# Kernel optimization log

Measured on AMD Instinct MI355X. Metric: run time of the kernel, lower is better.

## Reference

```python
import jax, jax.numpy as jnp
import numpy as np

WH, WW = 8, 8            # window_size
SH = 2                   # shuffle
NH = 6                   # num_heads
ED = 96                  # embed_dim
NP = WH * WW             # num_patches = 64
S2 = SH * SH             # shuffle group = 4
HD = ED // NH            # head_dim = 16
SCALE = HD ** -0.5 / SH
NW = 2048
NWM = 64
EPS = 1e-5


def _rel_pos_index():
    coords = np.stack(np.meshgrid(np.arange(WH), np.arange(WW), indexing='ij'))  # (2, wh, ww)
    cf = coords.reshape(2, -1)                                # (2, np)
    rel = (cf[:, :, None] - cf[:, None, :]).transpose(1, 2, 0).astype(np.int64)  # (np, np, 2)
    rel[..., 0] += WH - 1
    rel[..., 1] += WW - 1
    rel[..., 0] *= 2 * WW - 1
    return rel.sum(-1).reshape(-1)                            # (np*np,)

_REL_IDX = jnp.asarray(_rel_pos_index())


def setup_inputs() -> dict:
    key = jax.random.key(0)
    ks = jax.random.split(key, 6)
    return {
        'query': jax.random.normal(ks[0], (NW, NP * S2, ED), dtype=jnp.float32),
        'key': jax.random.normal(ks[1], (NW, NP * S2, ED), dtype=jnp.float32),
        'value': jax.random.normal(ks[2], (NW, NP * S2, ED), dtype=jnp.float32),
        'mask': jax.random.normal(ks[3], (NWM, NP, NP), dtype=jnp.float32),
        'bias_table': jax.random.normal(ks[4], (( 2 * WH - 1) * (2 * WW - 1), NH), dtype=jnp.float32) * 0.02,
        'norm_gamma': jnp.ones((S2, ED), dtype=jnp.float32),
        'norm_beta': jnp.zeros((S2, ED), dtype=jnp.float32),
        'proj_w': jax.random.normal(ks[5], (ED, ED), dtype=jnp.float32) * 0.02,
        'proj_b': jnp.zeros((ED,), dtype=jnp.float32),
    }


def reference(query, key, value, mask, bias_table, norm_gamma, norm_beta, proj_w, proj_b):
    nw = query.shape[0]

    def group(x):  # (nw, wh*sh*ww*sw, ed) -> (nw, np, s2, ed)
        x = x.reshape(nw, WH, SH, WW, SH, ED)
        return x.transpose(0, 1, 3, 2, 4, 5).reshape(nw, NP, S2, ED)

    q, k, v = group(query), group(key), group(value)

    # pre-norm LayerNorm over the joint (s2, ed) normalized shape
    mu = q.mean(axis=(-2, -1), keepdims=True)
    var = q.var(axis=(-2, -1), keepdims=True)
    q = (q - mu) / jnp.sqrt(var + EPS) * norm_gamma + norm_beta

    def heads(x):  # (nw, np, s2, ed) -> (nw, nh, np, s2, hd)
        return x.reshape(nw, NP, S2, NH, HD).transpose(0, 3, 1, 2, 4)

    q, k, v = heads(q), heads(k), heads(v)
    q = q * SCALE

    # QK^T contracting jointly over shuffle axis s and head_dim c
    attn = jnp.einsum('wnqsc,wnksc->wnqk', q, k)  # (nw, nh, np, np)

    bias = bias_table[_REL_IDX].reshape(NP, NP, NH).transpose(2, 0, 1)  # (nh, np, np)
    attn = attn + bias[None]

    nwm = mask.shape[0]
    b = nw // nwm
    attn = attn.reshape(b, nwm, NH, NP, NP) + mask[None, :, None]
    attn = jax.nn.softmax(attn.reshape(nw, NH, NP, NP), axis=-1)

    out = jnp.einsum('wnqk,wnksc->wnqsc', attn, v)  # (nw, nh, np, s2, hd)
    out = out.transpose(0, 2, 3, 1, 4).reshape(nw, NP, S2, ED)
    # group_partition_reversed
    out = out.reshape(nw, WH, WW, SH, SH, ED).transpose(0, 1, 3, 2, 4, 5).reshape(nw, NP * S2, ED)
    out = out @ proj_w.T + proj_b
    return out
```

## Files before the change

kernel.cpp:

```cpp
#include <hip/hip_runtime.h>
#include <hip/hip_bf16.h>


#define TPB 256

#define Q0   0
#define K0   8192
#define VT0  16384
#define PR0  24576
#define LDS_TOTAL 77824

typedef __attribute__((ext_vector_type(8))) short short8;
typedef __attribute__((ext_vector_type(4))) float f32x4;

union FRAG { uint4 u4; short8 s8; unsigned short us[8]; };

__device__ __forceinline__ int seq_of(int p, int s) {
    return ((p >> 3) << 5) | ((s >> 1) << 4) | ((p & 7) << 1) | (s & 1);
}

#define SWZ(row, slot) (((row) << 7) + ((((slot) ^ ((row) & 7))) << 4))

#define LGKM_FENCE() do { \
    asm volatile("s_waitcnt lgkmcnt(0)" ::: "memory"); \
    __builtin_amdgcn_sched_barrier(0); } while (0)

__device__ __forceinline__ unsigned short f2b(float x) {
    union { __hip_bfloat16 h; unsigned short u; } z;
    z.h = __float2bfloat16(x);
    return z.u;
}

__device__ __forceinline__ uint4 pack8(const float* v) {
    union { uint4 u4; unsigned short us[8]; } z;
#pragma unroll
    for (int i = 0; i < 8; ++i) z.us[i] = f2b(v[i]);
    return z.u4;
}

__device__ __forceinline__ void load_pack(const float* src, uint4* dst) {
    float v[16];
#pragma unroll
    for (int i = 0; i < 4; ++i) {
        float4 x = ((const float4*)src)[i];
        v[4 * i] = x.x; v[4 * i + 1] = x.y; v[4 * i + 2] = x.z; v[4 * i + 3] = x.w;
    }
    dst[0] = pack8(v);
    dst[1] = pack8(v + 8);
}

__global__ void build_comb(const float* __restrict__ gmask,
                           const float* __restrict__ gbt,
                           float* __restrict__ comb) {
    const int b = blockIdx.x;
    const int mi = b / 6, n = b - mi * 6;
    const int t = threadIdx.x;
    const float* mrow = gmask + (size_t)mi * 4096;
    float* crow = comb + (size_t)b * 4096;
#pragma unroll
    for (int e = 0; e < 4096; e += TPB) {
        const int i = e + t;
        const int q = i >> 6, k = i & 63;
        const int idx = ((q >> 3) - (k >> 3) + 7) * 15 + ((q & 7) - (k & 7) + 7);
        crow[i] = mrow[i] + gbt[idx * 6 + n];
    }
}

template <int USE_COMB>
__global__ __launch_bounds__(TPB, 2)
void dwa_mfma(const float* __restrict__ gq,
              const float* __restrict__ gk,
              const float* __restrict__ gv,
              const float* __restrict__ gmask,
              const float* __restrict__ gbt,
              const float* __restrict__ ggamma,
              const float* __restrict__ gbeta,
              const float* __restrict__ gpw,
              const float* __restrict__ gpb,
              float* __restrict__ gout,
              const float* __restrict__ comb,
              int nwm)
{
    __shared__ __align__(16) unsigned char Lraw[LDS_TOTAL];
    char* L = (char*)Lraw;

    const int w = blockIdx.x;
    const int t = threadIdx.x;
    const int lane = t & 63, wv = t >> 6;
    const int r15 = lane & 15, gsl = lane >> 4;

    const int p_a = t >> 2, s_a = t & 3;
    const int g_a = seq_of(p_a, s_a);
    const size_t rowbase = ((size_t)w * 256 + g_a) * 96;
    const int mbase = (w % nwm) * 4096;
    const int qr0 = (wv << 4) + (gsl << 2);
    const f32x4 zf = {0.f, 0.f, 0.f, 0.f};

    uint4 qreg[12];
    {
        float qv[96];
        float sum = 0.f, ssq = 0.f;
        const float4* qr4 = (const float4*)(gq + rowbase);
#pragma unroll
        for (int i = 0; i < 24; ++i) {
            float4 x = qr4[i];
            qv[4 * i] = x.x; qv[4 * i + 1] = x.y;
            qv[4 * i + 2] = x.z; qv[4 * i + 3] = x.w;
            sum += (x.x + x.y) + (x.z + x.w);
            ssq += (x.x * x.x + x.y * x.y) + (x.z * x.z + x.w * x.w);
        }
        sum += __shfl_xor(sum, 1); ssq += __shfl_xor(ssq, 1);
        sum += __shfl_xor(sum, 2); ssq += __shfl_xor(ssq, 2);
        const float mu = sum * (1.f / 384.f);
        const float rs = rsqrtf(ssq * (1.f / 384.f) - mu * mu + 1e-5f);
        const float4* ga4 = (const float4*)(ggamma + s_a * 96);
        const float4* be4 = (const float4*)(gbeta + s_a * 96);
#pragma unroll
        for (int c6 = 0; c6 < 6; ++c6) {
            float vals[16];
#pragma unroll
            for (int j = 0; j < 4; ++j) {
                float4 g = ga4[c6 * 4 + j];
                float4 b = be4[c6 * 4 + j];
                const int base = c6 * 16 + 4 * j;
                vals[4 * j + 0] = ((qv[base + 0] - mu) * rs * g.x + b.x) * 0.125f;
                vals[4 * j + 1] = ((qv[base + 1] - mu) * rs * g.y + b.y) * 0.125f;
                vals[4 * j + 2] = ((qv[base + 2] - mu) * rs * g.z + b.z) * 0.125f;
                vals[4 * j + 3] = ((qv[base + 3] - mu) * rs * g.w + b.w) * 0.125f;
            }
            qreg[2 * c6]     = pack8(vals);
            qreg[2 * c6 + 1] = pack8(vals + 8);
        }
    }

    uint4 kpf[2][2], vpf[2][2];
    load_pack(gk + rowbase, kpf[0]);
    load_pack(gv + rowbase, vpf[0]);

#pragma unroll
    for (int n = 0; n < 6; ++n) {
        *(uint4*)(L + Q0 + SWZ(p_a, s_a * 2))     = qreg[2 * n];
        *(uint4*)(L + Q0 + SWZ(p_a, s_a * 2 + 1)) = qreg[2 * n + 1];
        *(uint4*)(L + K0 + SWZ(p_a, s_a * 2))     = kpf[n & 1][0];
        *(uint4*)(L + K0 + SWZ(p_a, s_a * 2 + 1)) = kpf[n & 1][1];
#pragma unroll
        for (int h = 0; h < 2; ++h) {
            FRAG u; u.u4 = vpf[n & 1][h];
#pragma unroll
            for (int c = 0; c < 8; ++c) {
                const int np_ = s_a * 16 + h * 8 + c;
                *(unsigned short*)(L + VT0 + (np_ << 7) +
                    ((((p_a >> 3) ^ (np_ & 7))) << 4) + ((p_a & 7) << 1)) = u.us[c];
            }
        }
        if (n < 5) {
            load_pack(gk + rowbase + (n + 1) * 16, kpf[(n + 1) & 1]);
            load_pack(gv + rowbase + (n + 1) * 16, vpf[(n + 1) & 1]);
        }
        f32x4 sacc[4];
        if (USE_COMB) {
            const float* cb = comb + (size_t)((w % nwm) * 6 + n) * 4096;
#pragma unroll
            for (int tile = 0; tile < 4; ++tile)
#pragma unroll
                for (int r = 0; r < 4; ++r)
                    sacc[tile][r] = cb[((qr0 + r) << 6) + (tile << 4) + r15];
        } else {
#pragma unroll
            for (int tile = 0; tile < 4; ++tile) {
                const int kpx = (tile << 4) + r15;
                const int ik = kpx >> 3, jk = kpx & 7;
#pragma unroll
                for (int r = 0; r < 4; ++r) {
                    const int q = qr0 + r;
                    sacc[tile][r] = gbt[(((q >> 3) - ik + 7) * 15 + ((q & 7) - jk + 7)) * 6 + n]
                                  + gmask[mbase + (q << 6) + kpx];
                }
            }
        }
        __syncthreads();

        {
            FRAG a0, a1;
            a0.u4 = *(const uint4*)(L + Q0 + SWZ(wv * 16 + r15, gsl));
            a1.u4 = *(const uint4*)(L + Q0 + SWZ(wv * 16 + r15, 4 + gsl));
#pragma unroll
            for (int tile = 0; tile < 4; ++tile) {
                FRAG b0, b1;
                b0.u4 = *(const uint4*)(L + K0 + SWZ(tile * 16 + r15, gsl));
                b1.u4 = *(const uint4*)(L + K0 + SWZ(tile * 16 + r15, 4 + gsl));
                sacc[tile] = __builtin_amdgcn_mfma_f32_16x16x32_bf16(a0.s8, b0.s8, sacc[tile], 0, 0, 0);
                sacc[tile] = __builtin_amdgcn_mfma_f32_16x16x32_bf16(a1.s8, b1.s8, sacc[tile], 0, 0, 0);
            }
        }

#pragma unroll
        for (int r = 0; r < 4; ++r) {
            const int q = qr0 + r;
            float mx = fmaxf(fmaxf(sacc[0][r], sacc[1][r]),
                             fmaxf(sacc[2][r], sacc[3][r]));
            mx = fmaxf(mx, __shfl_xor(mx, 1));
            mx = fmaxf(mx, __shfl_xor(mx, 2));
            mx = fmaxf(mx, __shfl_xor(mx, 4));
            mx = fmaxf(mx, __shfl_xor(mx, 8));
            float sm = 0.f;
#pragma unroll
            for (int tile = 0; tile < 4; ++tile) {
                sacc[tile][r] = __expf(sacc[tile][r] - mx);
                sm += sacc[tile][r];
            }
            sm += __shfl_xor(sm, 1);
            sm += __shfl_xor(sm, 2);
            sm += __shfl_xor(sm, 4);
            sm += __shfl_xor(sm, 8);
            const float inv = 1.0f / sm;
#pragma unroll
            for (int tile = 0; tile < 4; ++tile) {
                const int col = (tile << 4) + r15;
                *(unsigned short*)(L + Q0 + (q << 7) +
                                   (((col >> 3) ^ (q & 7)) << 4) + ((col & 7) << 1))
                    = f2b(sacc[tile][r] * inv);
            }
        }
        LGKM_FENCE();

        f32x4 oacc[4];
        {
            FRAG pa0, pa1;
            pa0.u4 = *(const uint4*)(L + Q0 + SWZ(wv * 16 + r15, gsl));
            pa1.u4 = *(const uint4*)(L + Q0 + SWZ(wv * 16 + r15, 4 + gsl));
#pragma unroll
            for (int ct = 0; ct < 4; ++ct) {
                FRAG b0, b1;
                b0.u4 = *(const uint4*)(L + VT0 + SWZ(ct * 16 + r15, gsl));
                b1.u4 = *(const uint4*)(L + VT0 + SWZ(ct * 16 + r15, 4 + gsl));
                oacc[ct] = __builtin_amdgcn_mfma_f32_16x16x32_bf16(pa0.s8, b0.s8, zf, 0, 0, 0);
                oacc[ct] = __builtin_amdgcn_mfma_f32_16x16x32_bf16(pa1.s8, b1.s8, oacc[ct], 0, 0, 0);
            }
        }

#pragma unroll
        for (int ct = 0; ct < 4; ++ct)
#pragma unroll
            for (int r = 0; r < 4; ++r) {
                const int token = ((qr0 + r) << 2) + ct;
                *(unsigned short*)(L + PR0 + token * 208 + ((n << 4) + r15) * 2)
                    = f2b(oacc[ct][r]);
            }
        __syncthreads();
    }

    {
        FRAG bw[3][6];
#pragma unroll
        for (int kk = 0; kk < 3; ++kk)
#pragma unroll
            for (int ct = 0; ct < 6; ++ct) {
                const int o = (ct << 4) + r15;
                const float4* wp = (const float4*)(gpw + o * 96 + kk * 32 + (gsl << 3));
                float4 w0 = wp[0], w1 = wp[1];
                float w8[8] = {w0.x, w0.y, w0.z, w0.w, w1.x, w1.y, w1.z, w1.w};
                bw[kk][ct].u4 = pack8(w8);
            }
        float pbv[6];
#pragma unroll
        for (int ct = 0; ct < 6; ++ct) pbv[ct] = gpb[(ct << 4) + r15];

#pragma unroll
        for (int mt = 0; mt < 4; ++mt) {
            const int rowA = (wv << 6) + (mt << 4) + r15;
            FRAG A[3];
#pragma unroll
            for (int kk = 0; kk < 3; ++kk)
                A[kk].u4 = *(const uint4*)(L + PR0 + rowA * 208 + kk * 64 + (gsl << 4));
            f32x4 acc[6];
#pragma unroll
            for (int ct = 0; ct < 6; ++ct) {
                acc[ct] = __builtin_amdgcn_mfma_f32_16x16x32_bf16(A[0].s8, bw[0][ct].s8, zf, 0, 0, 0);
                acc[ct] = __builtin_amdgcn_mfma_f32_16x16x32_bf16(A[1].s8, bw[1][ct].s8, acc[ct], 0, 0, 0);
                acc[ct] = __builtin_amdgcn_mfma_f32_16x16x32_bf16(A[2].s8, bw[2][ct].s8, acc[ct], 0, 0, 0);
            }
#pragma unroll
            for (int ct = 0; ct < 6; ++ct)
#pragma unroll
                for (int rr = 0; rr < 4; ++rr) {
                    const int token = (wv << 6) + (mt << 4) + (gsl << 2) + rr;
                    const int p = token >> 2, s = token & 3;
                    const int gsq = seq_of(p, s);
                    gout[((size_t)w * 256 + gsq) * 96 + (ct << 4) + r15]
                        = acc[ct][rr] + pbv[ct];
                }
        }
    }
}

extern "C" void kernel_launch(void* const* d_in, const int* in_sizes, int n_in,
                              void* d_out, int out_size, void* d_ws, size_t ws_size,
                              hipStream_t stream) {
    const float* gq     = (const float*)d_in[0];
    const float* gk     = (const float*)d_in[1];
    const float* gv     = (const float*)d_in[2];
    const float* gmask  = (const float*)d_in[3];
    const float* gbt    = (const float*)d_in[4];
    const float* ggamma = (const float*)d_in[5];
    const float* gbeta  = (const float*)d_in[6];
    const float* gpw    = (const float*)d_in[7];
    const float* gpb    = (const float*)d_in[8];
    float* gout = (float*)d_out;

    const int nw  = in_sizes[0] / (256 * 96);
    const int nwm = in_sizes[3] / (64 * 64);
    const size_t comb_bytes = (size_t)nwm * 6 * 4096 * sizeof(float);

    if (ws_size >= comb_bytes) {
        float* comb = (float*)d_ws;
        build_comb<<<nwm * 6, TPB, 0, stream>>>(gmask, gbt, comb);
        dwa_mfma<1><<<nw, TPB, 0, stream>>>(gq, gk, gv, gmask, gbt, ggamma, gbeta,
                                            gpw, gpb, gout, comb, nwm);
    } else {
        dwa_mfma<0><<<nw, TPB, 0, stream>>>(gq, gk, gv, gmask, gbt, ggamma, gbeta,
                                            gpw, gpb, gout, (const float*)nullptr, nwm);
    }
}
```

Baseline: 274.1 us.

## Split fused attention kernel into attention and projection kernels via bf16 workspace

Splits the single fused kernel into an attention kernel that writes the per-head outputs as bf16 to a global workspace, and a separate projection kernel that reads them back and applies the output linear layer. The attention kernel drops its LDS footprint from 76KB to 24KB. It streams the Q LayerNorm per head slice instead of keeping all packed Q in registers, which allows higher occupancy (launch bounds raised to 5 blocks). The cost is an extra global round trip of the intermediate (about 2048*6*256*16 bf16) and an additional kernel launch. The old fused path remains as a fallback when the workspace is too small.

```diff
diff --git a/kernel.cpp b/kernel.cpp
--- a/kernel.cpp
+++ b/kernel.cpp
@@ -7,8 +7,7 @@
 #define Q0   0
 #define K0   8192
 #define VT0  16384
-#define PR0  24576
-#define LDS_TOTAL 77824
+#define ATTN_LDS 24576
 
 typedef __attribute__((ext_vector_type(8))) short short8;
 typedef __attribute__((ext_vector_type(4))) float f32x4;
@@ -23,6 +22,17 @@
 
 #define LGKM_FENCE() do { \
     asm volatile("s_waitcnt lgkmcnt(0)" ::: "memory"); \
+    __builtin_amdgcn_sched_barrier(0); } while (0)
+
+#define BAR_STAGE() do { \
+    asm volatile("s_waitcnt lgkmcnt(0)" ::: "memory"); \
+    __builtin_amdgcn_sched_barrier(0); \
+    __builtin_amdgcn_s_barrier(); \
+    __builtin_amdgcn_sched_barrier(0); } while (0)
+
+#define BAR_WAR() do { \
+    __builtin_amdgcn_sched_barrier(0); \
+    __builtin_amdgcn_s_barrier(); \
     __builtin_amdgcn_sched_barrier(0); } while (0)
 
 __device__ __forceinline__ unsigned short f2b(float x) {
@@ -44,6 +54,24 @@
     for (int i = 0; i < 4; ++i) {
         float4 x = ((const float4*)src)[i];
         v[4 * i] = x.x; v[4 * i + 1] = x.y; v[4 * i + 2] = x.z; v[4 * i + 3] = x.w;
+    }
+    dst[0] = pack8(v);
+    dst[1] = pack8(v + 8);
+}
+
+__device__ __forceinline__ void load_pack_qln(const float* src, const float* ga,
+                                              const float* be, float mu, float rs,
+                                              uint4* dst) {
+    float v[16];
+#pragma unroll
+    for (int i = 0; i < 4; ++i) {
+        float4 x = ((const float4*)src)[i];
+        float4 g = ((const float4*)ga)[i];
+        float4 b = ((const float4*)be)[i];
+        v[4 * i + 0] = ((x.x - mu) * rs * g.x + b.x) * 0.125f;
+        v[4 * i + 1] = ((x.y - mu) * rs * g.y + b.y) * 0.125f;
+        v[4 * i + 2] = ((x.z - mu) * rs * g.z + b.z) * 0.125f;
+        v[4 * i + 3] = ((x.w - mu) * rs * g.w + b.w) * 0.125f;
     }
     dst[0] = pack8(v);
     dst[1] = pack8(v + 8);
@@ -66,22 +94,17 @@
     }
 }
 
-template <int USE_COMB>
-__global__ __launch_bounds__(TPB, 2)
-void dwa_mfma(const float* __restrict__ gq,
+__global__ __launch_bounds__(TPB, 5)
+void dwa_attn(const float* __restrict__ gq,
               const float* __restrict__ gk,
               const float* __restrict__ gv,
-              const float* __restrict__ gmask,
-              const float* __restrict__ gbt,
               const float* __restrict__ ggamma,
               const float* __restrict__ gbeta,
-              const float* __restrict__ gpw,
-              const float* __restrict__ gpb,
-              float* __restrict__ gout,
               const float* __restrict__ comb,
+              __hip_bfloat16* __restrict__ gpre,
               int nwm)
 {
-    __shared__ __align__(16) unsigned char Lraw[LDS_TOTAL];
+    __shared__ __align__(16) unsigned char Lraw[ATTN_LDS];
     char* L = (char*)Lraw;
 
     const int w = blockIdx.x;
@@ -92,55 +115,36 @@
     const int p_a = t >> 2, s_a = t & 3;
     const int g_a = seq_of(p_a, s_a);
     const size_t rowbase = ((size_t)w * 256 + g_a) * 96;
-    const int mbase = (w % nwm) * 4096;
     const int qr0 = (wv << 4) + (gsl << 2);
     const f32x4 zf = {0.f, 0.f, 0.f, 0.f};
 
-    uint4 qreg[12];
+    float mu, rs;
     {
-        float qv[96];
+        const float4* qr4 = (const float4*)(gq + rowbase);
         float sum = 0.f, ssq = 0.f;
-        const float4* qr4 = (const float4*)(gq + rowbase);
 #pragma unroll
         for (int i = 0; i < 24; ++i) {
             float4 x = qr4[i];
-            qv[4 * i] = x.x; qv[4 * i + 1] = x.y;
-            qv[4 * i + 2] = x.z; qv[4 * i + 3] = x.w;
             sum += (x.x + x.y) + (x.z + x.w);
             ssq += (x.x * x.x + x.y * x.y) + (x.z * x.z + x.w * x.w);
         }
         sum += __shfl_xor(sum, 1); ssq += __shfl_xor(ssq, 1);
         sum += __shfl_xor(sum, 2); ssq += __shfl_xor(ssq, 2);
-        const float mu = sum * (1.f / 384.f);
-        const float rs = rsqrtf(ssq * (1.f / 384.f) - mu * mu + 1e-5f);
-        const float4* ga4 = (const float4*)(ggamma + s_a * 96);
-        const float4* be4 = (const float4*)(gbeta + s_a * 96);
-#pragma unroll
-        for (int c6 = 0; c6 < 6; ++c6) {
-            float vals[16];
-#pragma unroll
-            for (int j = 0; j < 4; ++j) {
-                float4 g = ga4[c6 * 4 + j];
-                float4 b = be4[c6 * 4 + j];
-                const int base = c6 * 16 + 4 * j;
-                vals[4 * j + 0] = ((qv[base + 0] - mu) * rs * g.x + b.x) * 0.125f;
-                vals[4 * j + 1] = ((qv[base + 1] - mu) * rs * g.y + b.y) * 0.125f;
-                vals[4 * j + 2] = ((qv[base + 2] - mu) * rs * g.z + b.z) * 0.125f;
-                vals[4 * j + 3] = ((qv[base + 3] - mu) * rs * g.w + b.w) * 0.125f;
-            }
-            qreg[2 * c6]     = pack8(vals);
-            qreg[2 * c6 + 1] = pack8(vals + 8);
-        }
-    }
-
-    uint4 kpf[2][2], vpf[2][2];
+        mu = sum * (1.f / 384.f);
+        rs = rsqrtf(ssq * (1.f / 384.f) - mu * mu + 1e-5f);
+    }
+    const float* gaT = ggamma + s_a * 96;
+    const float* beT = gbeta + s_a * 96;
+
+    uint4 qpf[2][2], kpf[2][2], vpf[2][2];
+    load_pack_qln(gq + rowbase, gaT, beT, mu, rs, qpf[0]);
     load_pack(gk + rowbase, kpf[0]);
     load_pack(gv + rowbase, vpf[0]);
 
 #pragma unroll
     for (int n = 0; n < 6; ++n) {
-        *(uint4*)(L + Q0 + SWZ(p_a, s_a * 2))     = qreg[2 * n];
-        *(uint4*)(L + Q0 + SWZ(p_a, s_a * 2 + 1)) = qreg[2 * n + 1];
+        *(uint4*)(L + Q0 + SWZ(p_a, s_a * 2))     = qpf[n & 1][0];
+        *(uint4*)(L + Q0 + SWZ(p_a, s_a * 2 + 1)) = qpf[n & 1][1];
         *(uint4*)(L + K0 + SWZ(p_a, s_a * 2))     = kpf[n & 1][0];
         *(uint4*)(L + K0 + SWZ(p_a, s_a * 2 + 1)) = kpf[n & 1][1];
 #pragma unroll
@@ -154,31 +158,22 @@
             }
         }
         if (n < 5) {
-            load_pack(gk + rowbase + (n + 1) * 16, kpf[(n + 1) & 1]);
-            load_pack(gv + rowbase + (n + 1) * 16, vpf[(n + 1) & 1]);
+            const int off = (n + 1) * 16;
+            load_pack_qln(gq + rowbase + off, gaT + off, beT + off, mu, rs,
+                          qpf[(n + 1) & 1]);
+            load_pack(gk + rowbase + off, kpf[(n + 1) & 1]);
+            load_pack(gv + rowbase + off, vpf[(n + 1) & 1]);
         }
         f32x4 sacc[4];
-        if (USE_COMB) {
+        {
             const float* cb = comb + (size_t)((w % nwm) * 6 + n) * 4096;
 #pragma unroll
             for (int tile = 0; tile < 4; ++tile)
 #pragma unroll
                 for (int r = 0; r < 4; ++r)
                     sacc[tile][r] = cb[((qr0 + r) << 6) + (tile << 4) + r15];
-        } else {
-#pragma unroll
-            for (int tile = 0; tile < 4; ++tile) {
-                const int kpx = (tile << 4) + r15;
-                const int ik = kpx >> 3, jk = kpx & 7;
-#pragma unroll
-                for (int r = 0; r < 4; ++r) {
-                    const int q = qr0 + r;
-                    sacc[tile][r] = gbt[(((q >> 3) - ik + 7) * 15 + ((q & 7) - jk + 7)) * 6 + n]
-                                  + gmask[mbase + (q << 6) + kpx];
-                }
-            }
-        }
-        __syncthreads();
+        }
+        BAR_STAGE();
 
         {
             FRAG a0, a1;
@@ -239,17 +234,264 @@
             }
         }
 
+        {
+            __hip_bfloat16* pb = gpre + (((size_t)w * 6 + n) << 12) + r15;
+#pragma unroll
+            for (int ct = 0; ct < 4; ++ct)
+#pragma unroll
+                for (int r = 0; r < 4; ++r) {
+                    const int tok = ((qr0 + r) << 2) + ct;
+                    union { __hip_bfloat16 h; unsigned short u; } z;
+                    z.u = f2b(oacc[ct][r]);
+                    pb[tok << 4] = z.h;
+                }
+        }
+        BAR_WAR();
+    }
+}
+
+__global__ __launch_bounds__(TPB, 4)
+void dwa_proj(const __hip_bfloat16* __restrict__ gpre,
+              const float* __restrict__ gpw,
+              const float* __restrict__ gpb,
+              float* __restrict__ gout)
+{
+    const int w = blockIdx.x;
+    const int t = threadIdx.x;
+    const int lane = t & 63, wv = t >> 6;
+    const int r15 = lane & 15, gsl = lane >> 4;
+    const f32x4 zf = {0.f, 0.f, 0.f, 0.f};
+
+    FRAG bw[3][6];
+#pragma unroll
+    for (int kk = 0; kk < 3; ++kk)
+#pragma unroll
+        for (int ct = 0; ct < 6; ++ct) {
+            const int o = (ct << 4) + r15;
+            const float4* wp = (const float4*)(gpw + o * 96 + kk * 32 + (gsl << 3));
+            float4 w0 = wp[0], w1 = wp[1];
+            float w8[8] = {w0.x, w0.y, w0.z, w0.w, w1.x, w1.y, w1.z, w1.w};
+            bw[kk][ct].u4 = pack8(w8);
+        }
+    float pbv[6];
+#pragma unroll
+    for (int ct = 0; ct < 6; ++ct) pbv[ct] = gpb[(ct << 4) + r15];
+
+#pragma unroll
+    for (int mt = 0; mt < 4; ++mt) {
+        const int rowA = (wv << 6) + (mt << 4) + r15;
+        FRAG A[3];
+#pragma unroll
+        for (int kk = 0; kk < 3; ++kk) {
+            const int n = kk * 2 + (gsl >> 1);
+            const int c0 = (gsl & 1) << 3;
+            A[kk].u4 = *(const uint4*)(gpre + (((size_t)w * 6 + n) << 12) +
+                                       (rowA << 4) + c0);
+        }
+        f32x4 acc[6];
+#pragma unroll
+        for (int ct = 0; ct < 6; ++ct) {
+            acc[ct] = __builtin_amdgcn_mfma_f32_16x16x32_bf16(A[0].s8, bw[0][ct].s8, zf, 0, 0, 0);
+            acc[ct] = __builtin_amdgcn_mfma_f32_16x16x32_bf16(A[1].s8, bw[1][ct].s8, acc[ct], 0, 0, 0);
+            acc[ct] = __builtin_amdgcn_mfma_f32_16x16x32_bf16(A[2].s8, bw[2][ct].s8, acc[ct], 0, 0, 0);
+        }
+#pragma unroll
+        for (int ct = 0; ct < 6; ++ct)
+#pragma unroll
+            for (int rr = 0; rr < 4; ++rr) {
+                const int token = (wv << 6) + (mt << 4) + (gsl << 2) + rr;
+                const int p = token >> 2, s = token & 3;
+                const int gsq = seq_of(p, s);
+                gout[((size_t)w * 256 + gsq) * 96 + (ct << 4) + r15]
+                    = acc[ct][rr] + pbv[ct];
+            }
+    }
+}
+
+#define FQ0   0
+#define FK0   8192
+#define FVT0  16384
+#define FPR0  24576
+#define F_LDS 77824
+
+template <int USE_COMB>
+__global__ __launch_bounds__(TPB, 2)
+void dwa_fused(const float* __restrict__ gq,
+               const float* __restrict__ gk,
+               const float* __restrict__ gv,
+               const float* __restrict__ gmask,
+               const float* __restrict__ gbt,
+               const float* __restrict__ ggamma,
+               const float* __restrict__ gbeta,
+               const float* __restrict__ gpw,
+               const float* __restrict__ gpb,
+               float* __restrict__ gout,
+               const float* __restrict__ comb,
+               int nwm)
+{
+    __shared__ __align__(16) unsigned char Lraw[F_LDS];
+    char* L = (char*)Lraw;
+
+    const int w = blockIdx.x;
+    const int t = threadIdx.x;
+    const int lane = t & 63, wv = t >> 6;
+    const int r15 = lane & 15, gsl = lane >> 4;
+
+    const int p_a = t >> 2, s_a = t & 3;
+    const int g_a = seq_of(p_a, s_a);
+    const size_t rowbase = ((size_t)w * 256 + g_a) * 96;
+    const int mbase = (w % nwm) * 4096;
+    const int qr0 = (wv << 4) + (gsl << 2);
+    const f32x4 zf = {0.f, 0.f, 0.f, 0.f};
+
+    uint4 qreg[12];
+    {
+        float qv[96];
+        float sum = 0.f, ssq = 0.f;
+        const float4* qr4 = (const float4*)(gq + rowbase);
+#pragma unroll
+        for (int i = 0; i < 24; ++i) {
+            float4 x = qr4[i];
+            qv[4 * i] = x.x; qv[4 * i + 1] = x.y;
+            qv[4 * i + 2] = x.z; qv[4 * i + 3] = x.w;
+            sum += (x.x + x.y) + (x.z + x.w);
+            ssq += (x.x * x.x + x.y * x.y) + (x.z * x.z + x.w * x.w);
+        }
+        sum += __shfl_xor(sum, 1); ssq += __shfl_xor(ssq, 1);
+        sum += __shfl_xor(sum, 2); ssq += __shfl_xor(ssq, 2);
+        const float mu = sum * (1.f / 384.f);
+        const float rs = rsqrtf(ssq * (1.f / 384.f) - mu * mu + 1e-5f);
+        const float4* ga4 = (const float4*)(ggamma + s_a * 96);
+        const float4* be4 = (const float4*)(gbeta + s_a * 96);
+#pragma unroll
+        for (int c6 = 0; c6 < 6; ++c6) {
+            float vals[16];
+#pragma unroll
+            for (int j = 0; j < 4; ++j) {
+                float4 g = ga4[c6 * 4 + j];
+                float4 b = be4[c6 * 4 + j];
+                const int base = c6 * 16 + 4 * j;
+                vals[4 * j + 0] = ((qv[base + 0] - mu) * rs * g.x + b.x) * 0.125f;
+                vals[4 * j + 1] = ((qv[base + 1] - mu) * rs * g.y + b.y) * 0.125f;
+                vals[4 * j + 2] = ((qv[base + 2] - mu) * rs * g.z + b.z) * 0.125f;
+                vals[4 * j + 3] = ((qv[base + 3] - mu) * rs * g.w + b.w) * 0.125f;
+            }
+            qreg[2 * c6]     = pack8(vals);
+            qreg[2 * c6 + 1] = pack8(vals + 8);
+        }
+    }
+    uint4 kpf[2][2], vpf[2][2];
+    load_pack(gk + rowbase, kpf[0]);
+    load_pack(gv + rowbase, vpf[0]);
+
+#pragma unroll
+    for (int n = 0; n < 6; ++n) {
+        *(uint4*)(L + FQ0 + SWZ(p_a, s_a * 2))     = qreg[2 * n];
+        *(uint4*)(L + FQ0 + SWZ(p_a, s_a * 2 + 1)) = qreg[2 * n + 1];
+        *(uint4*)(L + FK0 + SWZ(p_a, s_a * 2))     = kpf[n & 1][0];
+        *(uint4*)(L + FK0 + SWZ(p_a, s_a * 2 + 1)) = kpf[n & 1][1];
+#pragma unroll
+        for (int h = 0; h < 2; ++h) {
+            FRAG u; u.u4 = vpf[n & 1][h];
+#pragma unroll
+            for (int c = 0; c < 8; ++c) {
+                const int np_ = s_a * 16 + h * 8 + c;
+                *(unsigned short*)(L + FVT0 + (np_ << 7) +
+                    ((((p_a >> 3) ^ (np_ & 7))) << 4) + ((p_a & 7) << 1)) = u.us[c];
+            }
+        }
+        if (n < 5) {
+            load_pack(gk + rowbase + (n + 1) * 16, kpf[(n + 1) & 1]);
+            load_pack(gv + rowbase + (n + 1) * 16, vpf[(n + 1) & 1]);
+        }
+        f32x4 sacc[4];
+        if (USE_COMB) {
+            const float* cb = comb + (size_t)((w % nwm) * 6 + n) * 4096;
+#pragma unroll
+            for (int tile = 0; tile < 4; ++tile)
+#pragma unroll
+                for (int r = 0; r < 4; ++r)
+                    sacc[tile][r] = cb[((qr0 + r) << 6) + (tile << 4) + r15];
+        } else {
+#pragma unroll
+            for (int tile = 0; tile < 4; ++tile) {
+                const int kpx = (tile << 4) + r15;
+                const int ik = kpx >> 3, jk = kpx & 7;
+#pragma unroll
+                for (int r = 0; r < 4; ++r) {
+                    const int q = qr0 + r;
+                    sacc[tile][r] = gbt[(((q >> 3) - ik + 7) * 15 + ((q & 7) - jk + 7)) * 6 + n]
+                                  + gmask[mbase + (q << 6) + kpx];
+                }
+            }
+        }
+        __syncthreads();
+        {
+            FRAG a0, a1;
+            a0.u4 = *(const uint4*)(L + FQ0 + SWZ(wv * 16 + r15, gsl));
+            a1.u4 = *(const uint4*)(L + FQ0 + SWZ(wv * 16 + r15, 4 + gsl));
+#pragma unroll
+            for (int tile = 0; tile < 4; ++tile) {
+                FRAG b0, b1;
+                b0.u4 = *(const uint4*)(L + FK0 + SWZ(tile * 16 + r15, gsl));
+                b1.u4 = *(const uint4*)(L + FK0 + SWZ(tile * 16 + r15, 4 + gsl));
+                sacc[tile] = __builtin_amdgcn_mfma_f32_16x16x32_bf16(a0.s8, b0.s8, sacc[tile], 0, 0, 0);
+                sacc[tile] = __builtin_amdgcn_mfma_f32_16x16x32_bf16(a1.s8, b1.s8, sacc[tile], 0, 0, 0);
+            }
+        }
+#pragma unroll
+        for (int r = 0; r < 4; ++r) {
+            const int q = qr0 + r;
+            float mx = fmaxf(fmaxf(sacc[0][r], sacc[1][r]),
+                             fmaxf(sacc[2][r], sacc[3][r]));
+            mx = fmaxf(mx, __shfl_xor(mx, 1));
+            mx = fmaxf(mx, __shfl_xor(mx, 2));
+            mx = fmaxf(mx, __shfl_xor(mx, 4));
+            mx = fmaxf(mx, __shfl_xor(mx, 8));
+            float sm = 0.f;
+#pragma unroll
+            for (int tile = 0; tile < 4; ++tile) {
+                sacc[tile][r] = __expf(sacc[tile][r] - mx);
+                sm += sacc[tile][r];
+            }
+            sm += __shfl_xor(sm, 1);
+            sm += __shfl_xor(sm, 2);
+            sm += __shfl_xor(sm, 4);
+            sm += __shfl_xor(sm, 8);
+            const float inv = 1.0f / sm;
+#pragma unroll
+            for (int tile = 0; tile < 4; ++tile) {
+                const int col = (tile << 4) + r15;
+                *(unsigned short*)(L + FQ0 + (q << 7) +
+                                   (((col >> 3) ^ (q & 7)) << 4) + ((col & 7) << 1))
+                    = f2b(sacc[tile][r] * inv);
+            }
+        }
+        LGKM_FENCE();
+        f32x4 oacc[4];
+        {
+            FRAG pa0, pa1;
+            pa0.u4 = *(const uint4*)(L + FQ0 + SWZ(wv * 16 + r15, gsl));
+            pa1.u4 = *(const uint4*)(L + FQ0 + SWZ(wv * 16 + r15, 4 + gsl));
+#pragma unroll
+            for (int ct = 0; ct < 4; ++ct) {
+                FRAG b0, b1;
+                b0.u4 = *(const uint4*)(L + FVT0 + SWZ(ct * 16 + r15, gsl));
+                b1.u4 = *(const uint4*)(L + FVT0 + SWZ(ct * 16 + r15, 4 + gsl));
+                oacc[ct] = __builtin_amdgcn_mfma_f32_16x16x32_bf16(pa0.s8, b0.s8, zf, 0, 0, 0);
+                oacc[ct] = __builtin_amdgcn_mfma_f32_16x16x32_bf16(pa1.s8, b1.s8, oacc[ct], 0, 0, 0);
+            }
+        }
 #pragma unroll
         for (int ct = 0; ct < 4; ++ct)
 #pragma unroll
             for (int r = 0; r < 4; ++r) {
                 const int token = ((qr0 + r) << 2) + ct;
-                *(unsigned short*)(L + PR0 + token * 208 + ((n << 4) + r15) * 2)
+                *(unsigned short*)(L + FPR0 + token * 208 + ((n << 4) + r15) * 2)
                     = f2b(oacc[ct][r]);
             }
         __syncthreads();
     }
-
     {
         FRAG bw[3][6];
 #pragma unroll
@@ -265,14 +507,13 @@
         float pbv[6];
 #pragma unroll
         for (int ct = 0; ct < 6; ++ct) pbv[ct] = gpb[(ct << 4) + r15];
-
 #pragma unroll
         for (int mt = 0; mt < 4; ++mt) {
             const int rowA = (wv << 6) + (mt << 4) + r15;
             FRAG A[3];
 #pragma unroll
             for (int kk = 0; kk < 3; ++kk)
-                A[kk].u4 = *(const uint4*)(L + PR0 + rowA * 208 + kk * 64 + (gsl << 4));
+                A[kk].u4 = *(const uint4*)(L + FPR0 + rowA * 208 + kk * 64 + (gsl << 4));
             f32x4 acc[6];
 #pragma unroll
             for (int ct = 0; ct < 6; ++ct) {
@@ -311,14 +552,22 @@
     const int nw  = in_sizes[0] / (256 * 96);
     const int nwm = in_sizes[3] / (64 * 64);
     const size_t comb_bytes = (size_t)nwm * 6 * 4096 * sizeof(float);
-
-    if (ws_size >= comb_bytes) {
+    const size_t comb_pad   = (comb_bytes + 255) & ~(size_t)255;
+    const size_t pre_bytes  = (size_t)nw * 6 * 256 * 16 * sizeof(__hip_bfloat16);
+
+    if (ws_size >= comb_pad + pre_bytes) {
+        float* comb = (float*)d_ws;
+        __hip_bfloat16* gpre = (__hip_bfloat16*)((char*)d_ws + comb_pad);
+        build_comb<<<nwm * 6, TPB, 0, stream>>>(gmask, gbt, comb);
+        dwa_attn<<<nw, TPB, 0, stream>>>(gq, gk, gv, ggamma, gbeta, comb, gpre, nwm);
+        dwa_proj<<<nw, TPB, 0, stream>>>(gpre, gpw, gpb, gout);
+    } else if (ws_size >= comb_bytes) {
         float* comb = (float*)d_ws;
         build_comb<<<nwm * 6, TPB, 0, stream>>>(gmask, gbt, comb);
-        dwa_mfma<1><<<nw, TPB, 0, stream>>>(gq, gk, gv, gmask, gbt, ggamma, gbeta,
-                                            gpw, gpb, gout, comb, nwm);
+        dwa_fused<1><<<nw, TPB, 0, stream>>>(gq, gk, gv, gmask, gbt, ggamma, gbeta,
+                                             gpw, gpb, gout, comb, nwm);
     } else {
-        dwa_mfma<0><<<nw, TPB, 0, stream>>>(gq, gk, gv, gmask, gbt, ggamma, gbeta,
-                                            gpw, gpb, gout, (const float*)nullptr, nwm);
-    }
-}
+        dwa_fused<0><<<nw, TPB, 0, stream>>>(gq, gk, gv, gmask, gbt, ggamma, gbeta,
+                                             gpw, gpb, gout, (const float*)nullptr, nwm);
+    }
+}
```

After: 654.8 us. +138.9%, slower.

## Keep projection A-fragments in registers to shrink LDS and raise occupancy

Applied to the files above, without the earlier changes.

Instead of staging the whole per-head attention output (256 tokens x 96 channels bf16) in a large LDS buffer for the final projection, each head's output goes into a small 8 KB scratch area. Each lane then copies the bits it needs into a register-resident A fragment array for the projection MFMA. This shrinks LDS from about 76 KB to 32 KB per block and raises launch bounds from 2 to 3 blocks per CU. It also reorders the projection loop per output tile, and replaces __syncthreads with explicit barriers. The cost is 48 extra VGPRs for the A fragments, which may cause register pressure or spills under the tighter launch bound.

```diff
diff --git a/kernel.cpp b/kernel.cpp
--- a/kernel.cpp
+++ b/kernel.cpp
@@ -7,8 +7,8 @@
 #define Q0   0
 #define K0   8192
 #define VT0  16384
-#define PR0  24576
-#define LDS_TOTAL 77824
+#define PRS0 24576
+#define V8_LDS 32768
 
 typedef __attribute__((ext_vector_type(8))) short short8;
 typedef __attribute__((ext_vector_type(4))) float f32x4;
@@ -23,6 +23,17 @@
 
 #define LGKM_FENCE() do { \
     asm volatile("s_waitcnt lgkmcnt(0)" ::: "memory"); \
+    __builtin_amdgcn_sched_barrier(0); } while (0)
+
+#define BAR_STAGE() do { \
+    asm volatile("s_waitcnt lgkmcnt(0)" ::: "memory"); \
+    __builtin_amdgcn_sched_barrier(0); \
+    __builtin_amdgcn_s_barrier(); \
+    __builtin_amdgcn_sched_barrier(0); } while (0)
+
+#define BAR_WAR() do { \
+    __builtin_amdgcn_sched_barrier(0); \
+    __builtin_amdgcn_s_barrier(); \
     __builtin_amdgcn_sched_barrier(0); } while (0)
 
 __device__ __forceinline__ unsigned short f2b(float x) {
@@ -67,21 +78,21 @@
 }
 
 template <int USE_COMB>
-__global__ __launch_bounds__(TPB, 2)
-void dwa_mfma(const float* __restrict__ gq,
-              const float* __restrict__ gk,
-              const float* __restrict__ gv,
-              const float* __restrict__ gmask,
-              const float* __restrict__ gbt,
-              const float* __restrict__ ggamma,
-              const float* __restrict__ gbeta,
-              const float* __restrict__ gpw,
-              const float* __restrict__ gpb,
-              float* __restrict__ gout,
-              const float* __restrict__ comb,
-              int nwm)
+__global__ __launch_bounds__(TPB, 3)
+void dwa_v8(const float* __restrict__ gq,
+            const float* __restrict__ gk,
+            const float* __restrict__ gv,
+            const float* __restrict__ gmask,
+            const float* __restrict__ gbt,
+            const float* __restrict__ ggamma,
+            const float* __restrict__ gbeta,
+            const float* __restrict__ gpw,
+            const float* __restrict__ gpb,
+            float* __restrict__ gout,
+            const float* __restrict__ comb,
+            int nwm)
 {
-    __shared__ __align__(16) unsigned char Lraw[LDS_TOTAL];
+    __shared__ __align__(16) unsigned char Lraw[V8_LDS];
     char* L = (char*)Lraw;
 
     const int w = blockIdx.x;
@@ -132,10 +143,16 @@
             qreg[2 * c6 + 1] = pack8(vals + 8);
         }
     }
-
     uint4 kpf[2][2], vpf[2][2];
     load_pack(gk + rowbase, kpf[0]);
     load_pack(gv + rowbase, vpf[0]);
+
+    FRAG A[4][3];
+#pragma unroll
+    for (int mt = 0; mt < 4; ++mt)
+#pragma unroll
+        for (int kk = 0; kk < 3; ++kk)
+            A[mt][kk].u4 = make_uint4(0, 0, 0, 0);
 
 #pragma unroll
     for (int n = 0; n < 6; ++n) {
@@ -178,7 +195,7 @@
                 }
             }
         }
-        __syncthreads();
+        BAR_STAGE();
 
         {
             FRAG a0, a1;
@@ -243,53 +260,55 @@
         for (int ct = 0; ct < 4; ++ct)
 #pragma unroll
             for (int r = 0; r < 4; ++r) {
-                const int token = ((qr0 + r) << 2) + ct;
-                *(unsigned short*)(L + PR0 + token * 208 + ((n << 4) + r15) * 2)
-                    = f2b(oacc[ct][r]);
-            }
-        __syncthreads();
+                const int tok = ((qr0 + r) << 2) + ct;
+                *(unsigned short*)(L + PRS0 + ((r15 >> 3) << 12) + (tok << 4) +
+                                   ((r15 & 7) << 1)) = f2b(oacc[ct][r]);
+            }
+        LGKM_FENCE();
+
+        {
+            const bool keep = ((gsl >> 1) == (n & 1));
+            const int prsb = PRS0 + ((gsl & 1) << 12);
+#pragma unroll
+            for (int mt = 0; mt < 4; ++mt) {
+                const int tok = (wv << 6) + (mt << 4) + r15;
+                uint4 v = *(const uint4*)(L + prsb + (tok << 4));
+                A[mt][n >> 1].u4.x = keep ? v.x : A[mt][n >> 1].u4.x;
+                A[mt][n >> 1].u4.y = keep ? v.y : A[mt][n >> 1].u4.y;
+                A[mt][n >> 1].u4.z = keep ? v.z : A[mt][n >> 1].u4.z;
+                A[mt][n >> 1].u4.w = keep ? v.w : A[mt][n >> 1].u4.w;
+            }
+        }
+        BAR_WAR();
     }
 
     {
-        FRAG bw[3][6];
-#pragma unroll
-        for (int kk = 0; kk < 3; ++kk)
-#pragma unroll
-            for (int ct = 0; ct < 6; ++ct) {
-                const int o = (ct << 4) + r15;
+#pragma unroll
+        for (int ct = 0; ct < 6; ++ct) {
+            const int o = (ct << 4) + r15;
+            const float pbv = gpb[o];
+            FRAG bw[3];
+#pragma unroll
+            for (int kk = 0; kk < 3; ++kk) {
                 const float4* wp = (const float4*)(gpw + o * 96 + kk * 32 + (gsl << 3));
                 float4 w0 = wp[0], w1 = wp[1];
                 float w8[8] = {w0.x, w0.y, w0.z, w0.w, w1.x, w1.y, w1.z, w1.w};
-                bw[kk][ct].u4 = pack8(w8);
-            }
-        float pbv[6];
-#pragma unroll
-        for (int ct = 0; ct < 6; ++ct) pbv[ct] = gpb[(ct << 4) + r15];
-
-#pragma unroll
-        for (int mt = 0; mt < 4; ++mt) {
-            const int rowA = (wv << 6) + (mt << 4) + r15;
-            FRAG A[3];
-#pragma unroll
-            for (int kk = 0; kk < 3; ++kk)
-                A[kk].u4 = *(const uint4*)(L + PR0 + rowA * 208 + kk * 64 + (gsl << 4));
-            f32x4 acc[6];
-#pragma unroll
-            for (int ct = 0; ct < 6; ++ct) {
-                acc[ct] = __builtin_amdgcn_mfma_f32_16x16x32_bf16(A[0].s8, bw[0][ct].s8, zf, 0, 0, 0);
-                acc[ct] = __builtin_amdgcn_mfma_f32_16x16x32_bf16(A[1].s8, bw[1][ct].s8, acc[ct], 0, 0, 0);
-                acc[ct] = __builtin_amdgcn_mfma_f32_16x16x32_bf16(A[2].s8, bw[2][ct].s8, acc[ct], 0, 0, 0);
-            }
-#pragma unroll
-            for (int ct = 0; ct < 6; ++ct)
+                bw[kk].u4 = pack8(w8);
+            }
+#pragma unroll
+            for (int mt = 0; mt < 4; ++mt) {
+                f32x4 acc;
+                acc = __builtin_amdgcn_mfma_f32_16x16x32_bf16(A[mt][0].s8, bw[0].s8, zf, 0, 0, 0);
+                acc = __builtin_amdgcn_mfma_f32_16x16x32_bf16(A[mt][1].s8, bw[1].s8, acc, 0, 0, 0);
+                acc = __builtin_amdgcn_mfma_f32_16x16x32_bf16(A[mt][2].s8, bw[2].s8, acc, 0, 0, 0);
 #pragma unroll
                 for (int rr = 0; rr < 4; ++rr) {
                     const int token = (wv << 6) + (mt << 4) + (gsl << 2) + rr;
                     const int p = token >> 2, s = token & 3;
                     const int gsq = seq_of(p, s);
-                    gout[((size_t)w * 256 + gsq) * 96 + (ct << 4) + r15]
-                        = acc[ct][rr] + pbv[ct];
+                    gout[((size_t)w * 256 + gsq) * 96 + o] = acc[rr] + pbv;
                 }
+            }
         }
     }
 }
@@ -315,10 +334,10 @@
     if (ws_size >= comb_bytes) {
         float* comb = (float*)d_ws;
         build_comb<<<nwm * 6, TPB, 0, stream>>>(gmask, gbt, comb);
-        dwa_mfma<1><<<nw, TPB, 0, stream>>>(gq, gk, gv, gmask, gbt, ggamma, gbeta,
-                                            gpw, gpb, gout, comb, nwm);
+        dwa_v8<1><<<nw, TPB, 0, stream>>>(gq, gk, gv, gmask, gbt, ggamma, gbeta,
+                                          gpw, gpb, gout, comb, nwm);
     } else {
-        dwa_mfma<0><<<nw, TPB, 0, stream>>>(gq, gk, gv, gmask, gbt, ggamma, gbeta,
-                                            gpw, gpb, gout, (const float*)nullptr, nwm);
-    }
-}
+        dwa_v8<0><<<nw, TPB, 0, stream>>>(gq, gk, gv, gmask, gbt, ggamma, gbeta,
+                                          gpw, gpb, gout, (const float*)nullptr, nwm);
+    }
+}
```

Measured after the change: 621.4 us. +126.7%, slower.

## Compute transposed scores so softmax reduces in-lane and stores P vectorized

Applied to the files above, without the earlier changes.

The QK^T MFMA now puts K as the A operand and Q as B, so each lane holds one query's scores across 16 keys. The row max and sum then reduce mostly in registers with two cross-lane shuffles instead of four per row. This lets the probabilities go to LDS as packed 8-byte stores rather than scattered 2-byte stores. To match the new layout, the combined bias/mask table is written transposed (via an LDS transpose in build_comb), and the V-transpose swizzle changes to spread bank conflicts.

```diff
diff --git a/kernel.cpp b/kernel.cpp
--- a/kernel.cpp
+++ b/kernel.cpp
@@ -8,7 +8,7 @@
 #define K0   8192
 #define VT0  16384
 #define PR0  24576
-#define LDS_TOTAL 77824
+#define V_LDS 77824
 
 typedef __attribute__((ext_vector_type(8))) short short8;
 typedef __attribute__((ext_vector_type(4))) float f32x4;
@@ -20,6 +20,7 @@
 }
 
 #define SWZ(row, slot) (((row) << 7) + ((((slot) ^ ((row) & 7))) << 4))
+#define SVK(n) (((n) ^ ((n) >> 3)) & 7)
 
 #define LGKM_FENCE() do { \
     asm volatile("s_waitcnt lgkmcnt(0)" ::: "memory"); \
@@ -57,12 +58,19 @@
     const int t = threadIdx.x;
     const float* mrow = gmask + (size_t)mi * 4096;
     float* crow = comb + (size_t)b * 4096;
+    __shared__ float mt_[64 * 65];
 #pragma unroll
     for (int e = 0; e < 4096; e += TPB) {
         const int i = e + t;
-        const int q = i >> 6, k = i & 63;
+        mt_[(i >> 6) * 65 + (i & 63)] = mrow[i];
+    }
+    __syncthreads();
+#pragma unroll
+    for (int e = 0; e < 4096; e += TPB) {
+        const int i = e + t;
+        const int k = i >> 6, q = i & 63;
         const int idx = ((q >> 3) - (k >> 3) + 7) * 15 + ((q & 7) - (k & 7) + 7);
-        crow[i] = mrow[i] + gbt[idx * 6 + n];
+        crow[i] = mt_[q * 65 + k] + gbt[idx * 6 + n];
     }
 }
 
@@ -81,7 +89,7 @@
               const float* __restrict__ comb,
               int nwm)
 {
-    __shared__ __align__(16) unsigned char Lraw[LDS_TOTAL];
+    __shared__ __align__(16) unsigned char Lraw[V_LDS];
     char* L = (char*)Lraw;
 
     const int w = blockIdx.x;
@@ -94,6 +102,7 @@
     const size_t rowbase = ((size_t)w * 256 + g_a) * 96;
     const int mbase = (w % nwm) * 4096;
     const int qr0 = (wv << 4) + (gsl << 2);
+    const int qcol = (wv << 4) + r15;
     const f32x4 zf = {0.f, 0.f, 0.f, 0.f};
 
     uint4 qreg[12];
@@ -132,7 +141,6 @@
             qreg[2 * c6 + 1] = pack8(vals + 8);
         }
     }
-
     uint4 kpf[2][2], vpf[2][2];
     load_pack(gk + rowbase, kpf[0]);
     load_pack(gv + rowbase, vpf[0]);
@@ -150,7 +158,7 @@
             for (int c = 0; c < 8; ++c) {
                 const int np_ = s_a * 16 + h * 8 + c;
                 *(unsigned short*)(L + VT0 + (np_ << 7) +
-                    ((((p_a >> 3) ^ (np_ & 7))) << 4) + ((p_a & 7) << 1)) = u.us[c];
+                    (((p_a >> 3) ^ SVK(np_)) << 4) + ((p_a & 7) << 1)) = u.us[c];
             }
         }
         if (n < 5) {
@@ -159,67 +167,68 @@
         }
         f32x4 sacc[4];
         if (USE_COMB) {
-            const float* cb = comb + (size_t)((w % nwm) * 6 + n) * 4096;
-#pragma unroll
-            for (int tile = 0; tile < 4; ++tile)
+            const float* cb = comb + (size_t)((w % nwm) * 6 + n) * 4096 + qcol;
+#pragma unroll
+            for (int mt = 0; mt < 4; ++mt)
 #pragma unroll
                 for (int r = 0; r < 4; ++r)
-                    sacc[tile][r] = cb[((qr0 + r) << 6) + (tile << 4) + r15];
+                    sacc[mt][r] = cb[((mt << 4) + (gsl << 2) + r) << 6];
         } else {
-#pragma unroll
-            for (int tile = 0; tile < 4; ++tile) {
-                const int kpx = (tile << 4) + r15;
-                const int ik = kpx >> 3, jk = kpx & 7;
+            const int iq = qcol >> 3, jq = qcol & 7;
+#pragma unroll
+            for (int mt = 0; mt < 4; ++mt)
 #pragma unroll
                 for (int r = 0; r < 4; ++r) {
-                    const int q = qr0 + r;
-                    sacc[tile][r] = gbt[(((q >> 3) - ik + 7) * 15 + ((q & 7) - jk + 7)) * 6 + n]
-                                  + gmask[mbase + (q << 6) + kpx];
+                    const int k = (mt << 4) + (gsl << 2) + r;
+                    sacc[mt][r] = gbt[((iq - (k >> 3) + 7) * 15 + (jq - (k & 7) + 7)) * 6 + n]
+                                + gmask[mbase + (qcol << 6) + k];
                 }
-            }
         }
         __syncthreads();
 
         {
-            FRAG a0, a1;
-            a0.u4 = *(const uint4*)(L + Q0 + SWZ(wv * 16 + r15, gsl));
-            a1.u4 = *(const uint4*)(L + Q0 + SWZ(wv * 16 + r15, 4 + gsl));
-#pragma unroll
-            for (int tile = 0; tile < 4; ++tile) {
-                FRAG b0, b1;
-                b0.u4 = *(const uint4*)(L + K0 + SWZ(tile * 16 + r15, gsl));
-                b1.u4 = *(const uint4*)(L + K0 + SWZ(tile * 16 + r15, 4 + gsl));
-                sacc[tile] = __builtin_amdgcn_mfma_f32_16x16x32_bf16(a0.s8, b0.s8, sacc[tile], 0, 0, 0);
-                sacc[tile] = __builtin_amdgcn_mfma_f32_16x16x32_bf16(a1.s8, b1.s8, sacc[tile], 0, 0, 0);
-            }
-        }
-
-#pragma unroll
-        for (int r = 0; r < 4; ++r) {
-            const int q = qr0 + r;
-            float mx = fmaxf(fmaxf(sacc[0][r], sacc[1][r]),
-                             fmaxf(sacc[2][r], sacc[3][r]));
-            mx = fmaxf(mx, __shfl_xor(mx, 1));
-            mx = fmaxf(mx, __shfl_xor(mx, 2));
-            mx = fmaxf(mx, __shfl_xor(mx, 4));
-            mx = fmaxf(mx, __shfl_xor(mx, 8));
+            FRAG qf0, qf1;
+            qf0.u4 = *(const uint4*)(L + Q0 + SWZ(qcol, gsl));
+            qf1.u4 = *(const uint4*)(L + Q0 + SWZ(qcol, 4 + gsl));
+#pragma unroll
+            for (int mt = 0; mt < 4; ++mt) {
+                FRAG kf0, kf1;
+                kf0.u4 = *(const uint4*)(L + K0 + SWZ(mt * 16 + r15, gsl));
+                kf1.u4 = *(const uint4*)(L + K0 + SWZ(mt * 16 + r15, 4 + gsl));
+                sacc[mt] = __builtin_amdgcn_mfma_f32_16x16x32_bf16(kf0.s8, qf0.s8, sacc[mt], 0, 0, 0);
+                sacc[mt] = __builtin_amdgcn_mfma_f32_16x16x32_bf16(kf1.s8, qf1.s8, sacc[mt], 0, 0, 0);
+            }
+        }
+
+        {
+            float mx = sacc[0][0];
+#pragma unroll
+            for (int mt = 0; mt < 4; ++mt)
+#pragma unroll
+                for (int r = 0; r < 4; ++r) mx = fmaxf(mx, sacc[mt][r]);
+            mx = fmaxf(mx, __shfl_xor(mx, 16));
+            mx = fmaxf(mx, __shfl_xor(mx, 32));
             float sm = 0.f;
 #pragma unroll
-            for (int tile = 0; tile < 4; ++tile) {
-                sacc[tile][r] = __expf(sacc[tile][r] - mx);
-                sm += sacc[tile][r];
-            }
-            sm += __shfl_xor(sm, 1);
-            sm += __shfl_xor(sm, 2);
-            sm += __shfl_xor(sm, 4);
-            sm += __shfl_xor(sm, 8);
+            for (int mt = 0; mt < 4; ++mt)
+#pragma unroll
+                for (int r = 0; r < 4; ++r) {
+                    sacc[mt][r] = __expf(sacc[mt][r] - mx);
+                    sm += sacc[mt][r];
+                }
+            sm += __shfl_xor(sm, 16);
+            sm += __shfl_xor(sm, 32);
             const float inv = 1.0f / sm;
-#pragma unroll
-            for (int tile = 0; tile < 4; ++tile) {
-                const int col = (tile << 4) + r15;
-                *(unsigned short*)(L + Q0 + (q << 7) +
-                                   (((col >> 3) ^ (q & 7)) << 4) + ((col & 7) << 1))
-                    = f2b(sacc[tile][r] * inv);
+            const int qb = qcol << 7, qx = qcol & 7;
+#pragma unroll
+            for (int mt = 0; mt < 4; ++mt) {
+                unsigned u0 = (unsigned)f2b(sacc[mt][0] * inv)
+                            | ((unsigned)f2b(sacc[mt][1] * inv) << 16);
+                unsigned u1 = (unsigned)f2b(sacc[mt][2] * inv)
+                            | ((unsigned)f2b(sacc[mt][3] * inv) << 16);
+                const int slot = (mt << 1) + (gsl >> 1);
+                *(uint2*)(L + Q0 + qb + (((slot ^ qx)) << 4) + ((gsl & 1) << 3))
+                    = make_uint2(u0, u1);
             }
         }
         LGKM_FENCE();
@@ -227,13 +236,15 @@
         f32x4 oacc[4];
         {
             FRAG pa0, pa1;
-            pa0.u4 = *(const uint4*)(L + Q0 + SWZ(wv * 16 + r15, gsl));
-            pa1.u4 = *(const uint4*)(L + Q0 + SWZ(wv * 16 + r15, 4 + gsl));
+            pa0.u4 = *(const uint4*)(L + Q0 + SWZ(qcol, gsl));
+            pa1.u4 = *(const uint4*)(L + Q0 + SWZ(qcol, 4 + gsl));
 #pragma unroll
             for (int ct = 0; ct < 4; ++ct) {
+                const int nr = ct * 16 + r15;
+                const int sv = SVK(nr);
                 FRAG b0, b1;
-                b0.u4 = *(const uint4*)(L + VT0 + SWZ(ct * 16 + r15, gsl));
-                b1.u4 = *(const uint4*)(L + VT0 + SWZ(ct * 16 + r15, 4 + gsl));
+                b0.u4 = *(const uint4*)(L + VT0 + (nr << 7) + ((gsl ^ sv) << 4));
+                b1.u4 = *(const uint4*)(L + VT0 + (nr << 7) + (((4 + gsl) ^ sv) << 4));
                 oacc[ct] = __builtin_amdgcn_mfma_f32_16x16x32_bf16(pa0.s8, b0.s8, zf, 0, 0, 0);
                 oacc[ct] = __builtin_amdgcn_mfma_f32_16x16x32_bf16(pa1.s8, b1.s8, oacc[ct], 0, 0, 0);
             }
```

Result: slower. 410.0 us (+49.6%).
